# Kernel optimization log

Hardware: AMD Instinct MI355X
Metric: run time of the kernel (lower is better)

The kernel has to match this reference:

```python
import jax, jax.numpy as jnp
import numpy as np

EPS_BN = 1e-5
EPS_LN = 1e-5


def _conv1d(x, w, b, pad):
    # x: (B, Cin, L), w: (Cout, Cin, K)
    y = jax.lax.conv_general_dilated(x, w, window_strides=(1,), padding=[(pad, pad)],
                                     dimension_numbers=('NCH', 'OIH', 'NCH'))
    return y + b[None, :, None]


def _bn_eval(x, g, b, m, v):
    return (x - m[None, :, None]) * (g / jnp.sqrt(v + EPS_BN))[None, :, None] + b[None, :, None]


def _maxpool2(x):
    B, C, L = x.shape
    return x.reshape(B, C, L // 2, 2).max(-1)


def _wavelet(x, t, s, w):
    # x: (B, In); t, s, w: (Out, In); mexican_hat wavelet
    z = (x[:, None, :] - t[None]) / (s + 1e-8)  # (B, Out, In)
    wav = (1.0 - z * z) * jnp.exp(-0.5 * z * z)
    return jnp.einsum('boi,oi->bo', wav, w)


def _ln(x, g, b):
    m = x.mean(-1, keepdims=True)
    v = ((x - m) ** 2).mean(-1, keepdims=True)
    return (x - m) / jnp.sqrt(v + EPS_LN) * g + b


def setup_inputs() -> dict:
    key = jax.random.key(0)
    ks = iter(jax.random.split(key, 40))
    B, L = 1024, 1024
    R = 64                 # repr_dim
    KIN = 128 * (R // 4)   # 2048 = conv stem flattened features
    d = {}
    d['x'] = jax.random.normal(next(ks), (B, 1, L), jnp.float32)
    for i, (ci, co, k) in enumerate([(1, 32, 7), (32, 64, 5), (64, 128, 3)], 1):
        fan = ci * k
        d[f'conv{i}_w'] = jax.random.normal(next(ks), (co, ci, k), jnp.float32) / np.sqrt(fan)
        d[f'conv{i}_b'] = jnp.zeros((co,), jnp.float32)
        d[f'bn{i}_g'] = jnp.ones((co,), jnp.float32)
        d[f'bn{i}_b'] = jnp.zeros((co,), jnp.float32)
        d[f'bn{i}_m'] = jax.random.normal(next(ks), (co,), jnp.float32) * 0.1
        d[f'bn{i}_v'] = jax.random.uniform(next(ks), (co,), jnp.float32, 0.5, 1.5)
    for i, fin in enumerate([KIN, R, R], 1):
        d[f'wl{i}_t'] = jax.random.uniform(next(ks), (R, fin), jnp.float32, -1.0, 1.0)
        d[f'wl{i}_s'] = jax.random.uniform(next(ks), (R, fin), jnp.float32, 0.1, 1.0)
        d[f'wl{i}_w'] = jax.random.normal(next(ks), (R, fin), jnp.float32) / np.sqrt(fin)
        d[f'ln{i}_g'] = jnp.ones((R,), jnp.float32)
        d[f'ln{i}_b'] = jnp.zeros((R,), jnp.float32)
    return d


def _forward(x, p):
    h = _conv1d(x, p['conv1_w'], p['conv1_b'], 3)
    h = jax.nn.gelu(_bn_eval(h, p['bn1_g'], p['bn1_b'], p['bn1_m'], p['bn1_v']), approximate=False)
    h = _maxpool2(h)
    h = _conv1d(h, p['conv2_w'], p['conv2_b'], 2)
    h = jax.nn.gelu(_bn_eval(h, p['bn2_g'], p['bn2_b'], p['bn2_m'], p['bn2_v']), approximate=False)
    h = _maxpool2(h)
    h = _conv1d(h, p['conv3_w'], p['conv3_b'], 1)
    h = jax.nn.gelu(_bn_eval(h, p['bn3_g'], p['bn3_b'], p['bn3_m'], p['bn3_v']), approximate=False)
    # AdaptiveAvgPool1d(16): L=256 splits evenly into 16 bins of 16
    B, C, L = h.shape
    h = h.reshape(B, C, 16, L // 16).mean(-1)
    feat = h.reshape(B, -1)  # (B, 2048)
    for i in (1, 2, 3):
        feat = _ln(jax.nn.silu(_wavelet(feat, p[f'wl{i}_t'], p[f'wl{i}_s'], p[f'wl{i}_w'])),
                   p[f'ln{i}_g'], p[f'ln{i}_b'])
    return feat  # (B, 64)


def reference(x, conv1_w, conv1_b, bn1_g, bn1_b, bn1_m, bn1_v,
              conv2_w, conv2_b, bn2_g, bn2_b, bn2_m, bn2_v,
              conv3_w, conv3_b, bn3_g, bn3_b, bn3_m, bn3_v,
              wl1_t, wl1_s, wl1_w, ln1_g, ln1_b,
              wl2_t, wl2_s, wl2_w, ln2_g, ln2_b,
              wl3_t, wl3_s, wl3_w, ln3_g, ln3_b):
    p = dict(locals())
    p.pop('x')
    return _forward(x, p)
```

## Files before the change

kernel.cpp:

```cpp
#include <hip/hip_runtime.h>
#include <hip/hip_bf16.h>
#include <math.h>

#define WS_W2H   0
#define WS_W2L   5120
#define WS_W3H   10240
#define WS_W3L   23040
#define WS_A1    35840
#define WS_C1    35872
#define WS_A2    35904
#define WS_C2    35968
#define WS_A3    36032
#define WS_C3    36160
#define WS_T1H   36288
#define WS_WW1H  101824
#define WS_IS1T  167360
#define WS_T2T   298432
#define WS_IS2T  302528
#define WS_WW2T  306624
#define WS_T3T   310720
#define WS_IS3T  314816
#define WS_WW3T  318912
#define WS_FEAT  323008

typedef _Float16 f16x8 __attribute__((ext_vector_type(8)));
typedef _Float16 f16x4v __attribute__((ext_vector_type(4)));
typedef float    f32x4 __attribute__((ext_vector_type(4)));

struct InPtrs { const float* p[34]; };

__device__ __forceinline__ float gelu_fast(float x) {
    float z  = 0.70710678118654752f * x;
    float az = fabsf(z);
    float t  = __builtin_amdgcn_rcpf(fmaf(0.3275911f, az, 1.0f));
    float p  = fmaf(1.061405429f, t, -1.453152027f);
    p = fmaf(p, t, 1.421413741f);
    p = fmaf(p, t, -0.284496736f);
    p = fmaf(p, t, 0.254829592f);
    p = p * t;
    float e  = __expf(-z * z);
    float erf_abs = fmaf(-p, e, 1.0f);
    float erfv = copysignf(erf_abs, z);
    return 0.5f * x * (1.0f + erfv);
}

__global__ __launch_bounds__(256) void prep_kernel(InPtrs in, float* __restrict__ ws) {
    int idx = blockIdx.x * 256 + threadIdx.x;
    if (idx >= 453856) return;
    if (idx < 10240) {
        int co = idx / 160; int kk = idx - co * 160;
        int tap = kk >> 5, ci = kk & 31;
        float val = in.p[7][co * 160 + ci * 5 + tap];
        _Float16 hi = (_Float16)val;
        ((_Float16*)(ws + WS_W2H))[co * 160 + kk] = hi;
        ((_Float16*)(ws + WS_W2L))[co * 160 + kk] = (_Float16)(val - (float)hi);
    } else if (idx < 35840) {
        int n = idx - 10240;
        int co = n / 200; int k = n - co * 200;
        float val = 0.0f;
        if (k < 192) { int ci = k & 63; int tap = k >> 6; val = in.p[13][co * 192 + ci * 3 + tap]; }
        _Float16 hi = (_Float16)val;
        ((_Float16*)(ws + WS_W3H))[co * 200 + k] = hi;
        ((_Float16*)(ws + WS_W3L))[co * 200 + k] = (_Float16)(val - (float)hi);
    } else if (idx < 36064) {
        int n = idx - 35840;
        int ch, offA, offC; const float *cb, *g, *bb, *m, *v;
        if (n < 32)      { ch = n;      cb = in.p[2];  g = in.p[3];  bb = in.p[4];  m = in.p[5];  v = in.p[6];  offA = WS_A1; offC = WS_C1; }
        else if (n < 96) { ch = n - 32; cb = in.p[8];  g = in.p[9];  bb = in.p[10]; m = in.p[11]; v = in.p[12]; offA = WS_A2; offC = WS_C2; }
        else             { ch = n - 96; cb = in.p[14]; g = in.p[15]; bb = in.p[16]; m = in.p[17]; v = in.p[18]; offA = WS_A3; offC = WS_C3; }
        float A = g[ch] * rsqrtf(v[ch] + 1e-5f);
        ws[offA + ch] = A;
        ws[offC + ch] = (cb[ch] - m[ch]) * A + bb[ch];
    } else if (idx < 429280) {
        int n = idx - 36064;
        int arr = n / 131072; int m = n - arr * 131072;
        int o = m >> 11; int i = m & 2047;
        float val = in.p[19 + arr][o * 2048 + i];
        int pidx = ((i >> 2) * 64 + o) * 4 + (i & 3);
        if (arr == 0)      ((_Float16*)(ws + WS_T1H))[pidx]  = (_Float16)val;
        else if (arr == 1) ws[WS_IS1T + pidx] = 1.0f / (val + 1e-8f);
        else               ((_Float16*)(ws + WS_WW1H))[pidx] = (_Float16)val;
    } else {
        int n = idx - 429280;
        int layer = n / 12288; int m = n - layer * 12288;
        int arr = m / 4096; int mm = m - arr * 4096;
        int o = mm >> 6; int i = mm & 63;
        float val = in.p[(layer == 0 ? 24 : 29) + arr][o * 64 + i];
        if (arr == 1) val = 1.0f / (val + 1e-8f);
        int base;
        if (layer == 0) base = (arr == 0) ? WS_T2T : (arr == 1) ? WS_IS2T : WS_WW2T;
        else            base = (arr == 0) ? WS_T3T : (arr == 1) ? WS_IS3T : WS_WW3T;
        ws[base + ((i >> 2) * 64 + o) * 4 + (i & 3)] = val;
    }
}

__global__ __launch_bounds__(256) void kconv_kernel(const float* __restrict__ x,
                                                    const float* __restrict__ w1,
                                                    const float* __restrict__ ws,
                                                    const _Float16* __restrict__ w3h,
                                                    const _Float16* __restrict__ w3l,
                                                    float* __restrict__ feat) {
    __shared__ __align__(16) float xs[560];
    __shared__ float w1s[224];
    __shared__ float a1s[32], c1s[32], a2s[64], c2s[64];
    __shared__ __align__(16) _Float16 U[276 * 40];

    _Float16* h1s = U;

    int t = threadIdx.x;
    int b = blockIdx.x >> 1, q = blockIdx.x & 1;

    for (int j = t; j < 560; j += 256) {
        int gx = 512 * q - 11 + j;
        xs[j] = (gx >= 0 && gx < 1024) ? x[b * 1024 + gx] : 0.0f;
    }
    if (t < 224) w1s[t] = w1[t];
    if (t < 32) { a1s[t] = ws[WS_A1 + t]; c1s[t] = ws[WS_C1 + t]; }
    if (t < 64) { a2s[t] = ws[WS_A2 + t]; c2s[t] = ws[WS_C2 + t]; }
    __syncthreads();

    for (int item = t; item < 32 * 69; item += 256) {
        int rq = item >> 5, ci = item & 31;
        const float4* xp = (const float4*)(xs + 8 * rq);
        float4 X0 = xp[0], X1 = xp[1], X2 = xp[2], X3 = xp[3];
        float f[16] = {X0.x, X0.y, X0.z, X0.w, X1.x, X1.y, X1.z, X1.w,
                       X2.x, X2.y, X2.z, X2.w, X3.x, X3.y, X3.z, X3.w};
        float wk0 = w1s[ci * 7],     wk1 = w1s[ci * 7 + 1], wk2 = w1s[ci * 7 + 2];
        float wk3 = w1s[ci * 7 + 3], wk4 = w1s[ci * 7 + 4], wk5 = w1s[ci * 7 + 5];
        float wk6 = w1s[ci * 7 + 6];
        float A = a1s[ci], C = c1s[ci];
        #pragma unroll
        for (int r4 = 0; r4 < 4; ++r4) {
            int r = 4 * rq + r4;
            int hp = 256 * q - 4 + r;
            float val = 0.0f;
            if ((unsigned)hp < 512u) {
                int j = 2 * r4;
                float d0 = f[j]*wk0 + f[j+1]*wk1 + f[j+2]*wk2 + f[j+3]*wk3
                         + f[j+4]*wk4 + f[j+5]*wk5 + f[j+6]*wk6;
                float d1 = f[j+1]*wk0 + f[j+2]*wk1 + f[j+3]*wk2 + f[j+4]*wk3
                         + f[j+5]*wk4 + f[j+6]*wk5 + f[j+7]*wk6;
                val = fmaxf(gelu_fast(fmaf(d0, A, C)), gelu_fast(fmaf(d1, A, C)));
            }
            if (r < 276) h1s[r * 40 + ci] = (_Float16)val;
        }
    }
    __syncthreads();

    int w = t >> 6, lane = t & 63;
    int m = lane & 15, quad = lane >> 4;

    const _Float16* w2h = (const _Float16*)(ws + WS_W2H);
    const _Float16* w2l = (const _Float16*)(ws + WS_W2L);
    f32x4 acc[5][4] = {};

    #pragma unroll
    for (int s = 0; s < 5; ++s) {
        f16x8 bh[4], bl[4];
        #pragma unroll
        for (int tc = 0; tc < 4; ++tc) {
            int off = (16 * tc + m) * 160 + 32 * s + quad * 8;
            bh[tc] = *(const f16x8*)(w2h + off);
            bl[tc] = *(const f16x8*)(w2l + off);
        }
        #pragma unroll
        for (int i = 0; i < 5; ++i) {
            if (i == 4 && w != 0) continue;
            int fr = (i < 4) ? (4 * i + w) : 16;
            f16x8 ah = *(const f16x8*)(&h1s[(16 * fr + m + s) * 40 + quad * 8]);
            #pragma unroll
            for (int tc = 0; tc < 4; ++tc) {
                acc[i][tc] = __builtin_amdgcn_mfma_f32_16x16x32_f16(ah, bh[tc], acc[i][tc], 0, 0, 0);
                acc[i][tc] = __builtin_amdgcn_mfma_f32_16x16x32_f16(ah, bl[tc], acc[i][tc], 0, 0, 0);
            }
        }
    }
    __syncthreads();

    _Float16* h2s = U;
    if (q == 0 && t < 64) h2s[0 * 72 + t]   = (_Float16)0.f;
    if (q == 1 && t < 64) h2s[129 * 72 + t] = (_Float16)0.f;

    #pragma unroll
    for (int i = 0; i < 5; ++i) {
        if (i == 4 && w != 0) continue;
        int fr = (i < 4) ? (4 * i + w) : 16;
        #pragma unroll
        for (int tc = 0; tc < 4; ++tc) {
            int co = 16 * tc + m;
            float A2 = a2s[co], C2 = c2s[co];
            float g0 = gelu_fast(fmaf(acc[i][tc][0], A2, C2));
            float g1 = gelu_fast(fmaf(acc[i][tc][1], A2, C2));
            float g2 = gelu_fast(fmaf(acc[i][tc][2], A2, C2));
            float g3 = gelu_fast(fmaf(acc[i][tc][3], A2, C2));
            float p0 = fmaxf(g0, g1), p1 = fmaxf(g2, g3);
            int ll0 = 8 * fr + 2 * quad;
            int lg0 = 128 * q - 1 + ll0;
            if (ll0 < 130 && (unsigned)lg0 < 256u) h2s[ll0 * 72 + co] = (_Float16)p0;
            int ll1 = ll0 + 1, lg1 = lg0 + 1;
            if (ll1 < 130 && (unsigned)lg1 < 256u) h2s[ll1 * 72 + co] = (_Float16)p1;
        }
    }
    __syncthreads();

    int wr = w >> 1, wc = w & 1;
    f32x4 acc2[4][4] = {};
    size_t boff = (size_t)(wc * 64 + m) * 200 + quad * 8;

    #pragma unroll
    for (int s = 0; s < 6; ++s) {
        int kbase = s * 32;
        int k = kbase + quad * 8;
        int koff = k >> 6, ci = k & 63;
        f16x8 ah[4], bh[4], bl[4];
        #pragma unroll
        for (int tr = 0; tr < 4; ++tr) {
            int row = 64 * wr + 16 * tr + m;
            ah[tr] = *(const f16x8*)(&h2s[(row + koff) * 72 + ci]);
        }
        #pragma unroll
        for (int tc = 0; tc < 4; ++tc) {
            bh[tc] = *(const f16x8*)(w3h + boff + 16 * tc * 200 + kbase);
            bl[tc] = *(const f16x8*)(w3l + boff + 16 * tc * 200 + kbase);
        }
        #pragma unroll
        for (int tr = 0; tr < 4; ++tr)
            #pragma unroll
            for (int tc = 0; tc < 4; ++tc) {
                acc2[tr][tc] = __builtin_amdgcn_mfma_f32_16x16x32_f16(ah[tr], bh[tc], acc2[tr][tc], 0, 0, 0);
                acc2[tr][tc] = __builtin_amdgcn_mfma_f32_16x16x32_f16(ah[tr], bl[tc], acc2[tr][tc], 0, 0, 0);
            }
    }

    #pragma unroll
    for (int tc = 0; tc < 4; ++tc) {
        int co = 64 * wc + 16 * tc + m;
        float A3 = ws[WS_A3 + co], C3 = ws[WS_C3 + co];
        #pragma unroll
        for (int tr = 0; tr < 4; ++tr) {
            float s = 0.0f;
            #pragma unroll
            for (int r = 0; r < 4; ++r)
                s += gelu_fast(fmaf(acc2[tr][tc][r], A3, C3));
            s += __shfl_xor(s, 16, 64);
            s += __shfl_xor(s, 32, 64);
            if (quad == 0) {
                int bin = 8 * q + 4 * wr + tr;
                feat[(size_t)b * 2048 + co * 16 + bin] = s * 0.0625f;
            }
        }
    }
}

__device__ __forceinline__ float wave_sum(float v) {
    #pragma unroll
    for (int off = 32; off > 0; off >>= 1) v += __shfl_xor(v, off, 64);
    return v;
}
__device__ __forceinline__ float silu_f(float v) {
    return v / (1.0f + __expf(-v));
}
__device__ __forceinline__ float mexh(float x, float tv, float sv, float wv) {
    float z = (x - tv) * sv, z2 = z * z;
    return (1.0f - z2) * __expf(-0.5f * z2) * wv;
}

__global__ __launch_bounds__(1024) void k4_kernel(const float* __restrict__ ws,
        const float* __restrict__ ln1g, const float* __restrict__ ln1b,
        const float* __restrict__ ln2g, const float* __restrict__ ln2b,
        const float* __restrict__ ln3g, const float* __restrict__ ln3b,
        float* __restrict__ out) {
    __shared__ __align__(16) float fs[4 * 2048];
    __shared__ float red[16 * 256];

    int t = threadIdx.x;
    int b0 = blockIdx.x * 4;
    int o = t & 63, grp = t >> 6;
    const float* feat = ws + WS_FEAT;
    const f16x4v* t1p  = (const f16x4v*)(ws + WS_T1H);
    const f16x4v* w1p  = (const f16x4v*)(ws + WS_WW1H);
    const f32x4*  is1p = (const f32x4*)(ws + WS_IS1T);

    int g0 = grp * 32;
    f16x4v tv = t1p[g0 * 64 + o];
    f16x4v wv = w1p[g0 * 64 + o];
    f32x4  sv = is1p[g0 * 64 + o];

    {
        const float4* src = (const float4*)(feat + (size_t)b0 * 2048);
        float4* dst = (float4*)fs;
        for (int i = t; i < 2048; i += 1024) dst[i] = src[i];
    }
    __syncthreads();

    float acc0 = 0.0f, acc1 = 0.0f, acc2 = 0.0f, acc3 = 0.0f;
    for (int k = 0; k < 32; ++k) {
        int gi = g0 + k;
        f16x4v tn = t1p[(gi + 1) * 64 + o];
        f16x4v wn = w1p[(gi + 1) * 64 + o];
        f32x4  sn = is1p[(gi + 1) * 64 + o];
        f32x4 f0 = *(const f32x4*)(&fs[4 * gi]);
        f32x4 f1 = *(const f32x4*)(&fs[2048 + 4 * gi]);
        f32x4 f2 = *(const f32x4*)(&fs[4096 + 4 * gi]);
        f32x4 f3 = *(const f32x4*)(&fs[6144 + 4 * gi]);
        #pragma unroll
        for (int j = 0; j < 4; ++j) {
            float tj = (float)tv[j], wj = (float)wv[j], sj = sv[j];
            acc0 += mexh(f0[j], tj, sj, wj);
            acc1 += mexh(f1[j], tj, sj, wj);
            acc2 += mexh(f2[j], tj, sj, wj);
            acc3 += mexh(f3[j], tj, sj, wj);
        }
        tv = tn; sv = sn; wv = wn;
    }
    red[grp * 256 + 0 * 64 + o] = acc0;
    red[grp * 256 + 1 * 64 + o] = acc1;
    red[grp * 256 + 2 * 64 + o] = acc2;
    red[grp * 256 + 3 * 64 + o] = acc3;
    __syncthreads();

    if (grp < 4) {
        int w = grp;
        float y = 0.0f;
        #pragma unroll
        for (int j = 0; j < 16; ++j) y += red[j * 256 + w * 64 + o];

        y = silu_f(y);
        float m = wave_sum(y) * 0.015625f;
        float d = y - m;
        float var = wave_sum(d * d) * 0.015625f;
        float yn = d * rsqrtf(var + 1e-5f) * ln1g[o] + ln1b[o];

        {
            const f32x4* t2p  = (const f32x4*)(ws + WS_T2T);
            const f32x4* is2p = (const f32x4*)(ws + WS_IS2T);
            const f32x4* w2p  = (const f32x4*)(ws + WS_WW2T);
            f32x4 tc = t2p[o], sc = is2p[o], wc = w2p[o];
            float a = 0.0f;
            for (int g = 0; g < 16; ++g) {
                f32x4 tn = t2p[(g + 1) * 64 + o];
                f32x4 sn = is2p[(g + 1) * 64 + o];
                f32x4 wn = w2p[(g + 1) * 64 + o];
                #pragma unroll
                for (int j = 0; j < 4; ++j)
                    a += mexh(__shfl(yn, 4 * g + j, 64), tc[j], sc[j], wc[j]);
                tc = tn; sc = sn; wc = wn;
            }
            float y2 = silu_f(a);
            float m2 = wave_sum(y2) * 0.015625f;
            float d2 = y2 - m2;
            float v2 = wave_sum(d2 * d2) * 0.015625f;
            yn = d2 * rsqrtf(v2 + 1e-5f) * ln2g[o] + ln2b[o];
        }
        {
            const f32x4* t3p  = (const f32x4*)(ws + WS_T3T);
            const f32x4* is3p = (const f32x4*)(ws + WS_IS3T);
            const f32x4* w3p  = (const f32x4*)(ws + WS_WW3T);
            f32x4 tc = t3p[o], sc = is3p[o], wc = w3p[o];
            float a = 0.0f;
            for (int g = 0; g < 16; ++g) {
                f32x4 tn = t3p[(g + 1) * 64 + o];
                f32x4 sn = is3p[(g + 1) * 64 + o];
                f32x4 wn = w3p[(g + 1) * 64 + o];
                #pragma unroll
                for (int j = 0; j < 4; ++j)
                    a += mexh(__shfl(yn, 4 * g + j, 64), tc[j], sc[j], wc[j]);
                tc = tn; sc = sn; wc = wn;
            }
            float y3 = silu_f(a);
            float m3 = wave_sum(y3) * 0.015625f;
            float d3 = y3 - m3;
            float v3 = wave_sum(d3 * d3) * 0.015625f;
            yn = d3 * rsqrtf(v3 + 1e-5f) * ln3g[o] + ln3b[o];
        }
        out[((size_t)b0 + w) * 64 + o] = yn;
    }
}

extern "C" void kernel_launch(void* const* d_in, const int* in_sizes, int n_in,
                              void* d_out, int out_size, void* d_ws, size_t ws_size,
                              hipStream_t stream) {
    float* ws = (float*)d_ws;
    InPtrs ip;
    for (int i = 0; i < 34; ++i) ip.p[i] = (const float*)d_in[i];

    prep_kernel<<<1774, 256, 0, stream>>>(ip, ws);
    kconv_kernel<<<2048, 256, 0, stream>>>((const float*)d_in[0], (const float*)d_in[1],
                                           ws,
                                           (const _Float16*)(ws + WS_W3H),
                                           (const _Float16*)(ws + WS_W3L),
                                           ws + WS_FEAT);
    k4_kernel<<<256, 1024, 0, stream>>>(ws,
        (const float*)d_in[22], (const float*)d_in[23],
        (const float*)d_in[27], (const float*)d_in[28],
        (const float*)d_in[32], (const float*)d_in[33],
        (float*)d_out);
}
```

Measured before the change: 281.4 us.

## Split conv2/conv3 MFMA output columns into two passes to cut accumulator registers

The conv2 and conv3 MFMA stages now process their output-channel tiles in two sequential groups of two instead of all four at once. This halves the live accumulator arrays, which should lower VGPR pressure and may allow higher occupancy. To make that possible, the shared h1/h2 union buffer is split into two separate LDS arrays so conv2 can write h2 while h1 is still being read. The trade-offs are extra LDS use, reloading A fragments for each pass, and less MFMA work in flight per pass.

```diff
diff --git a/kernel.cpp b/kernel.cpp
--- a/kernel.cpp
+++ b/kernel.cpp
@@ -103,9 +103,8 @@
     __shared__ __align__(16) float xs[560];
     __shared__ float w1s[224];
     __shared__ float a1s[32], c1s[32], a2s[64], c2s[64];
-    __shared__ __align__(16) _Float16 U[276 * 40];
-
-    _Float16* h1s = U;
+    __shared__ __align__(16) _Float16 h1s[276 * 40];
+    __shared__ __align__(16) _Float16 h2s[130 * 72];
 
     int t = threadIdx.x;
     int b = blockIdx.x >> 1, q = blockIdx.x & 1;
@@ -117,6 +116,8 @@
     if (t < 224) w1s[t] = w1[t];
     if (t < 32) { a1s[t] = ws[WS_A1 + t]; c1s[t] = ws[WS_C1 + t]; }
     if (t < 64) { a2s[t] = ws[WS_A2 + t]; c2s[t] = ws[WS_C2 + t]; }
+    if (q == 0 && t < 64) h2s[0 * 72 + t]   = (_Float16)0.f;
+    if (q == 1 && t < 64) h2s[129 * 72 + t] = (_Float16)0.f;
     __syncthreads();
 
     for (int item = t; item < 32 * 69; item += 256) {
@@ -152,101 +153,101 @@
 
     const _Float16* w2h = (const _Float16*)(ws + WS_W2H);
     const _Float16* w2l = (const _Float16*)(ws + WS_W2L);
-    f32x4 acc[5][4] = {};
-
-    #pragma unroll
-    for (int s = 0; s < 5; ++s) {
-        f16x8 bh[4], bl[4];
-        #pragma unroll
-        for (int tc = 0; tc < 4; ++tc) {
-            int off = (16 * tc + m) * 160 + 32 * s + quad * 8;
-            bh[tc] = *(const f16x8*)(w2h + off);
-            bl[tc] = *(const f16x8*)(w2l + off);
+
+    #pragma unroll 1
+    for (int tcg = 0; tcg < 2; ++tcg) {
+        f32x4 acc[5][2] = {};
+        #pragma unroll
+        for (int s = 0; s < 5; ++s) {
+            f16x8 bh[2], bl[2];
+            #pragma unroll
+            for (int tcl = 0; tcl < 2; ++tcl) {
+                int off = (16 * (2 * tcg + tcl) + m) * 160 + 32 * s + quad * 8;
+                bh[tcl] = *(const f16x8*)(w2h + off);
+                bl[tcl] = *(const f16x8*)(w2l + off);
+            }
+            #pragma unroll
+            for (int i = 0; i < 5; ++i) {
+                if (i == 4 && w != 0) continue;
+                int fr = (i < 4) ? (4 * i + w) : 16;
+                f16x8 ah = *(const f16x8*)(&h1s[(16 * fr + m + s) * 40 + quad * 8]);
+                #pragma unroll
+                for (int tcl = 0; tcl < 2; ++tcl) {
+                    acc[i][tcl] = __builtin_amdgcn_mfma_f32_16x16x32_f16(ah, bh[tcl], acc[i][tcl], 0, 0, 0);
+                    acc[i][tcl] = __builtin_amdgcn_mfma_f32_16x16x32_f16(ah, bl[tcl], acc[i][tcl], 0, 0, 0);
+                }
+            }
         }
         #pragma unroll
         for (int i = 0; i < 5; ++i) {
             if (i == 4 && w != 0) continue;
             int fr = (i < 4) ? (4 * i + w) : 16;
-            f16x8 ah = *(const f16x8*)(&h1s[(16 * fr + m + s) * 40 + quad * 8]);
-            #pragma unroll
-            for (int tc = 0; tc < 4; ++tc) {
-                acc[i][tc] = __builtin_amdgcn_mfma_f32_16x16x32_f16(ah, bh[tc], acc[i][tc], 0, 0, 0);
-                acc[i][tc] = __builtin_amdgcn_mfma_f32_16x16x32_f16(ah, bl[tc], acc[i][tc], 0, 0, 0);
-            }
-        }
-    }
-    __syncthreads();
-
-    _Float16* h2s = U;
-    if (q == 0 && t < 64) h2s[0 * 72 + t]   = (_Float16)0.f;
-    if (q == 1 && t < 64) h2s[129 * 72 + t] = (_Float16)0.f;
-
-    #pragma unroll
-    for (int i = 0; i < 5; ++i) {
-        if (i == 4 && w != 0) continue;
-        int fr = (i < 4) ? (4 * i + w) : 16;
-        #pragma unroll
-        for (int tc = 0; tc < 4; ++tc) {
-            int co = 16 * tc + m;
-            float A2 = a2s[co], C2 = c2s[co];
-            float g0 = gelu_fast(fmaf(acc[i][tc][0], A2, C2));
-            float g1 = gelu_fast(fmaf(acc[i][tc][1], A2, C2));
-            float g2 = gelu_fast(fmaf(acc[i][tc][2], A2, C2));
-            float g3 = gelu_fast(fmaf(acc[i][tc][3], A2, C2));
-            float p0 = fmaxf(g0, g1), p1 = fmaxf(g2, g3);
-            int ll0 = 8 * fr + 2 * quad;
-            int lg0 = 128 * q - 1 + ll0;
-            if (ll0 < 130 && (unsigned)lg0 < 256u) h2s[ll0 * 72 + co] = (_Float16)p0;
-            int ll1 = ll0 + 1, lg1 = lg0 + 1;
-            if (ll1 < 130 && (unsigned)lg1 < 256u) h2s[ll1 * 72 + co] = (_Float16)p1;
+            #pragma unroll
+            for (int tcl = 0; tcl < 2; ++tcl) {
+                int co = 16 * (2 * tcg + tcl) + m;
+                float A2 = a2s[co], C2 = c2s[co];
+                float g0 = gelu_fast(fmaf(acc[i][tcl][0], A2, C2));
+                float g1 = gelu_fast(fmaf(acc[i][tcl][1], A2, C2));
+                float g2 = gelu_fast(fmaf(acc[i][tcl][2], A2, C2));
+                float g3 = gelu_fast(fmaf(acc[i][tcl][3], A2, C2));
+                float p0 = fmaxf(g0, g1), p1 = fmaxf(g2, g3);
+                int ll0 = 8 * fr + 2 * quad;
+                int lg0 = 128 * q - 1 + ll0;
+                if (ll0 < 130 && (unsigned)lg0 < 256u) h2s[ll0 * 72 + co] = (_Float16)p0;
+                int ll1 = ll0 + 1, lg1 = lg0 + 1;
+                if (ll1 < 130 && (unsigned)lg1 < 256u) h2s[ll1 * 72 + co] = (_Float16)p1;
+            }
         }
     }
     __syncthreads();
 
     int wr = w >> 1, wc = w & 1;
-    f32x4 acc2[4][4] = {};
-    size_t boff = (size_t)(wc * 64 + m) * 200 + quad * 8;
-
-    #pragma unroll
-    for (int s = 0; s < 6; ++s) {
-        int kbase = s * 32;
-        int k = kbase + quad * 8;
-        int koff = k >> 6, ci = k & 63;
-        f16x8 ah[4], bh[4], bl[4];
-        #pragma unroll
-        for (int tr = 0; tr < 4; ++tr) {
-            int row = 64 * wr + 16 * tr + m;
-            ah[tr] = *(const f16x8*)(&h2s[(row + koff) * 72 + ci]);
-        }
-        #pragma unroll
-        for (int tc = 0; tc < 4; ++tc) {
-            bh[tc] = *(const f16x8*)(w3h + boff + 16 * tc * 200 + kbase);
-            bl[tc] = *(const f16x8*)(w3l + boff + 16 * tc * 200 + kbase);
-        }
-        #pragma unroll
-        for (int tr = 0; tr < 4; ++tr)
-            #pragma unroll
-            for (int tc = 0; tc < 4; ++tc) {
-                acc2[tr][tc] = __builtin_amdgcn_mfma_f32_16x16x32_f16(ah[tr], bh[tc], acc2[tr][tc], 0, 0, 0);
-                acc2[tr][tc] = __builtin_amdgcn_mfma_f32_16x16x32_f16(ah[tr], bl[tc], acc2[tr][tc], 0, 0, 0);
-            }
-    }
-
-    #pragma unroll
-    for (int tc = 0; tc < 4; ++tc) {
-        int co = 64 * wc + 16 * tc + m;
-        float A3 = ws[WS_A3 + co], C3 = ws[WS_C3 + co];
-        #pragma unroll
-        for (int tr = 0; tr < 4; ++tr) {
-            float s = 0.0f;
-            #pragma unroll
-            for (int r = 0; r < 4; ++r)
-                s += gelu_fast(fmaf(acc2[tr][tc][r], A3, C3));
-            s += __shfl_xor(s, 16, 64);
-            s += __shfl_xor(s, 32, 64);
-            if (quad == 0) {
-                int bin = 8 * q + 4 * wr + tr;
-                feat[(size_t)b * 2048 + co * 16 + bin] = s * 0.0625f;
+
+    #pragma unroll 1
+    for (int tcg = 0; tcg < 2; ++tcg) {
+        f32x4 acc2[4][2] = {};
+        size_t boff = (size_t)(wc * 64 + m) * 200 + quad * 8;
+        #pragma unroll
+        for (int s = 0; s < 6; ++s) {
+            int kbase = s * 32;
+            int k = kbase + quad * 8;
+            int koff = k >> 6, ci = k & 63;
+            f16x8 ah[4], bh[2], bl[2];
+            #pragma unroll
+            for (int tr = 0; tr < 4; ++tr) {
+                int row = 64 * wr + 16 * tr + m;
+                ah[tr] = *(const f16x8*)(&h2s[(row + koff) * 72 + ci]);
+            }
+            #pragma unroll
+            for (int tcl = 0; tcl < 2; ++tcl) {
+                int tc = 2 * tcg + tcl;
+                bh[tcl] = *(const f16x8*)(w3h + boff + 16 * tc * 200 + kbase);
+                bl[tcl] = *(const f16x8*)(w3l + boff + 16 * tc * 200 + kbase);
+            }
+            #pragma unroll
+            for (int tr = 0; tr < 4; ++tr)
+                #pragma unroll
+                for (int tcl = 0; tcl < 2; ++tcl) {
+                    acc2[tr][tcl] = __builtin_amdgcn_mfma_f32_16x16x32_f16(ah[tr], bh[tcl], acc2[tr][tcl], 0, 0, 0);
+                    acc2[tr][tcl] = __builtin_amdgcn_mfma_f32_16x16x32_f16(ah[tr], bl[tcl], acc2[tr][tcl], 0, 0, 0);
+                }
+        }
+        #pragma unroll
+        for (int tcl = 0; tcl < 2; ++tcl) {
+            int co = 64 * wc + 16 * (2 * tcg + tcl) + m;
+            float A3 = ws[WS_A3 + co], C3 = ws[WS_C3 + co];
+            #pragma unroll
+            for (int tr = 0; tr < 4; ++tr) {
+                float s = 0.0f;
+                #pragma unroll
+                for (int r = 0; r < 4; ++r)
+                    s += gelu_fast(fmaf(acc2[tr][tcl][r], A3, C3));
+                s += __shfl_xor(s, 16, 64);
+                s += __shfl_xor(s, 32, 64);
+                if (quad == 0) {
+                    int bin = 8 * q + 4 * wr + tr;
+                    feat[(size_t)b * 2048 + co * 16 + bin] = s * 0.0625f;
+                }
             }
         }
     }
```

Result: slower. 289.4 us (+2.8%).
